# Kernel tuning notes

Hardware: AMD Instinct MI355X
Metric: run time of the kernel (lower is better)

The kernel has to match this reference:

```python
import jax, jax.numpy as jnp
import numpy as np

N = 20000      # nodes (all graphs in batch)
E = 320000     # edges (avg degree 16)
G = 16         # graphs in batch
D_IN = 32      # raw node feature dim
D_LAP = 16     # laplacian PE dim
D = 256        # d_model
H = 8          # heads
DH = D // H    # head dim
L = 2          # encoder layers
D_FF = 2 * D   # FFN hidden (FFN_layer1: d_model -> 2*d_model)
EPS = 1e-5


def _layer_norm(x, g, b):
    m = jnp.mean(x, axis=-1, keepdims=True)
    v = jnp.var(x, axis=-1, keepdims=True)
    return g * (x - m) * jax.lax.rsqrt(v + EPS) + b


def setup_inputs() -> dict:
    key = jax.random.key(0)
    ks = jax.random.split(key, 32)

    feat = jax.random.normal(ks[0], (N, D_IN), dtype=jnp.float32)
    lap_pos = jax.random.normal(ks[1], (N, D_LAP), dtype=jnp.float32)
    # random +-1 sign flip per PE dim (done with torch.rand in the original forward)
    sign_flip = jnp.where(jax.random.uniform(ks[2], (D_LAP,)) >= 0.5, 1.0, -1.0).astype(jnp.float32)

    src = jax.random.randint(ks[3], (E,), 0, N, dtype=jnp.int32)
    dst = jax.random.randint(ks[4], (E,), 0, N, dtype=jnp.int32)
    graph_ids = jnp.sort(jax.random.randint(ks[5], (N,), 0, G, dtype=jnp.int32))

    def xavier(k, shape):
        fan_in, fan_out = shape[-2], shape[-1]
        lim = np.sqrt(6.0 / (fan_in + fan_out))
        return jax.random.uniform(k, shape, minval=-lim, maxval=lim, dtype=jnp.float32)

    inp = {
        "feat": feat, "lap_pos": lap_pos, "sign_flip": sign_flip,
        "src": src, "dst": dst, "graph_ids": graph_ids,
        # input embeddings
        "Wh": xavier(ks[6], (D_IN, D)), "bh": jnp.zeros((D,), jnp.float32),
        "Wlp": xavier(ks[7], (D_LAP, D)), "blp": jnp.zeros((D,), jnp.float32),
        # per-layer params, stacked on leading layer axis
        "Wq": xavier(ks[8], (L, D, D)), "Wk": xavier(ks[9], (L, D, D)),
        "Wv": xavier(ks[10], (L, D, D)),
        "Wo": xavier(ks[11], (L, D, D)), "bo": jnp.zeros((L, D), jnp.float32),
        "g1": jnp.ones((L, D), jnp.float32), "b1": jnp.zeros((L, D), jnp.float32),
        "W1": xavier(ks[12], (L, D, D_FF)), "c1": jnp.zeros((L, D_FF), jnp.float32),
        "W2": xavier(ks[13], (L, D_FF, D)), "c2": jnp.zeros((L, D), jnp.float32),
        "g2": jnp.ones((L, D), jnp.float32), "b2": jnp.zeros((L, D), jnp.float32),
    }
    return inp


def _forward(feat, lap_pos, sign_flip, src, dst, graph_ids,
             Wh, bh, Wlp, blp, Wq, Wk, Wv, Wo, bo, g1, b1, W1, c1, W2, c2, g2, b2):
    scale = np.sqrt(DH).astype(np.float32)

    h = feat @ Wh + bh                                  # [N, D]
    h = h + (lap_pos * sign_flip[None, :]) @ Wlp + blp  # add PE embedding

    for l in range(L):
        h_in1 = h
        Q = (h @ Wq[l]).reshape(N, H, DH)
        K = (h @ Wk[l]).reshape(N, H, DH)
        V = (h @ Wv[l]).reshape(N, H, DH)

        # per-edge dot-product score, then exp(clamp(score/sqrt(dh), -5, 5))
        score = jnp.sum(K[src] * Q[dst], axis=-1)                       # [E, H]
        s = jnp.exp(jnp.clip(score / scale, -5.0, 5.0))                # [E, H]

        # segment softmax of s over incoming edges per dst node (F.softmax on mailbox)
        m = jax.ops.segment_max(s, dst, num_segments=N)                 # [N, H], -inf if no in-edges
        p = jnp.exp(s - m[dst])                                         # [E, H]
        den = jax.ops.segment_sum(p, dst, num_segments=N)               # [N, H]
        msg = jax.ops.segment_sum(p[:, :, None] * V[src], dst, num_segments=N)  # [N, H, DH]
        attn = msg / jnp.where(den > 0, den, 1.0)[:, :, None]
        attn = attn.reshape(N, D)

        h = _layer_norm(h_in1 + attn @ Wo[l] + bo[l], g1[l], b1[l])
        h_in2 = h
        ff = jax.nn.relu(h @ W1[l] + c1[l]) @ W2[l] + c2[l]
        h = _layer_norm(h_in2 + ff, g2[l], b2[l])

    # mean readout per graph
    counts = jax.ops.segment_sum(jnp.ones((N,), h.dtype), graph_ids, num_segments=G)
    sums = jax.ops.segment_sum(h, graph_ids, num_segments=G)            # [G, D]
    return sums / jnp.where(counts > 0, counts, 1.0)[:, None]


def reference(feat, lap_pos, sign_flip, src, dst, graph_ids,
              Wh, bh, Wlp, blp, Wq, Wk, Wv, Wo, bo, g1, b1, W1, c1, W2, c2, g2, b2):
    return _forward(feat, lap_pos, sign_flip, src, dst, graph_ids,
                    Wh, bh, Wlp, blp, Wq, Wk, Wv, Wo, bo, g1, b1, W1, c1, W2, c2, g2, b2)
```

## Files before the change

### kernel.cpp

```cpp
#include <hip/hip_runtime.h>
#include <hip/hip_bf16.h>

#define NN   20000
#define EE   320000
#define GG   16
#define DD   256
#define HH   8
#define DHH  32
#define LLAYERS 2
#define DFF  512
#define DIN  32
#define DLAP 16
#define RSPLITS 16

typedef __attribute__((ext_vector_type(8))) short bf16x8;
typedef __attribute__((ext_vector_type(4))) float f32x4;

__device__ __forceinline__ void gld_lds16(const void* g, void* l) {
  __builtin_amdgcn_global_load_lds((const __attribute__((address_space(1))) uint32_t*)g,
                                   (__attribute__((address_space(3))) uint32_t*)l, 16, 0, 0);
}

__device__ __forceinline__ float b2f(unsigned short s) {
  union { unsigned int i; float f; } u;
  u.i = ((unsigned int)s) << 16;
  return u.f;
}

__device__ __forceinline__ unsigned short f2bu(float f) {
  __hip_bfloat16 b = __float2bfloat16(f);
  return *(unsigned short*)&b;
}

__global__ __launch_bounds__(256) void k_embed(
    const float* __restrict__ feat, const float* __restrict__ lap,
    const float* __restrict__ sign, const float* __restrict__ Wh,
    const float* __restrict__ bh, const float* __restrict__ Wlp,
    const float* __restrict__ blp, float* __restrict__ h,
    __hip_bfloat16* __restrict__ hb) {
  int n = blockIdx.x;
  int d = threadIdx.x;
  float acc = bh[d] + blp[d];
  const float* frow = feat + (size_t)n * DIN;
  const float* lrow = lap + (size_t)n * DLAP;
#pragma unroll
  for (int k = 0; k < DIN; ++k) acc += frow[k] * Wh[k * DD + d];
#pragma unroll
  for (int k = 0; k < DLAP; ++k) acc += (lrow[k] * sign[k]) * Wlp[k * DD + d];
  h[(size_t)n * DD + d] = acc;
  hb[(size_t)n * DD + d] = __float2bfloat16(acc);
}

__global__ __launch_bounds__(256) void k_wt(
    const float* __restrict__ in, __hip_bfloat16* __restrict__ out, int K, int N) {
  __shared__ float tile[32][33];
  const float* inl = in + (size_t)blockIdx.z * K * N;
  __hip_bfloat16* outl = out + (size_t)blockIdx.z * N * K;
  int bx = blockIdx.x;
  int by = blockIdx.y;
  int tx = threadIdx.x & 31, ty = threadIdx.x >> 5;
#pragma unroll
  for (int i = 0; i < 32; i += 8)
    tile[ty + i][tx] = inl[(size_t)(by * 32 + ty + i) * N + bx * 32 + tx];
  __syncthreads();
#pragma unroll
  for (int i = 0; i < 32; i += 8)
    outl[(size_t)(bx * 32 + ty + i) * K + by * 32 + tx] = __float2bfloat16(tile[tx][ty + i]);
}

template <bool BIAS, bool RELU, bool OUTBF16>
__global__ __launch_bounds__(256) void gemm_mfma(
    const __hip_bfloat16* __restrict__ A,
    const __hip_bfloat16* __restrict__ Bt0, const __hip_bfloat16* __restrict__ Bt1,
    const __hip_bfloat16* __restrict__ Bt2,
    const float* __restrict__ bias,
    void* __restrict__ C0, void* __restrict__ C1, void* __restrict__ C2,
    int M, int Ncols, int K) {
  const __hip_bfloat16* Bt = (blockIdx.z == 0) ? Bt0 : (blockIdx.z == 1) ? Bt1 : Bt2;
  void* Cout = (blockIdx.z == 0) ? C0 : (blockIdx.z == 1) ? C1 : C2;

  __shared__ short lA[2][4][128][8];
  __shared__ short lB[2][4][128][8];

  const int t = threadIdx.x;
  const int lane = t & 63, w = t >> 6;
  const int bm = blockIdx.x * 128, bn = blockIdx.y * 128;
  const int wr = w >> 1, wc = w & 1;
  const int fr = lane & 15, fg = lane >> 4;

  f32x4 acc[4][4] = {};

  auto stage = [&](int buf, int kt) {
    const int k0 = kt * 32;
#pragma unroll
    for (int it = 0; it < 2; ++it) {
      const int cbase = it * 256 + w * 64;
      const int c = cbase + lane;
      const int g = c >> 7, r = c & 127;
      int arow = bm + r;
      if (arow >= M) arow = M - 1;
      gld_lds16(A + (size_t)arow * K + k0 + g * 8,
                (short*)lA + ((size_t)buf * 4 * 128 + cbase) * 8);
      gld_lds16(Bt + (size_t)(bn + r) * K + k0 + g * 8,
                (short*)lB + ((size_t)buf * 4 * 128 + cbase) * 8);
    }
  };

  const int nt = K >> 5;
  stage(0, 0);
  for (int kt = 0; kt < nt; ++kt) {
    const int buf = kt & 1;
    __syncthreads();
    if (kt + 1 < nt) stage(buf ^ 1, kt + 1);
    bf16x8 af[4], bfr[4];
#pragma unroll
    for (int i = 0; i < 4; ++i)
      af[i] = *(const bf16x8*)&lA[buf][fg][wr * 64 + i * 16 + fr][0];
#pragma unroll
    for (int j = 0; j < 4; ++j)
      bfr[j] = *(const bf16x8*)&lB[buf][fg][wc * 64 + j * 16 + fr][0];
#pragma unroll
    for (int i = 0; i < 4; ++i)
#pragma unroll
      for (int j = 0; j < 4; ++j)
        acc[i][j] = __builtin_amdgcn_mfma_f32_16x16x32_bf16(af[i], bfr[j], acc[i][j], 0, 0, 0);
  }

#pragma unroll
  for (int i = 0; i < 4; ++i) {
    const int row0 = bm + wr * 64 + i * 16 + fg * 4;
#pragma unroll
    for (int j = 0; j < 4; ++j) {
      const int col = bn + wc * 64 + j * 16 + fr;
      float bv = BIAS ? bias[col] : 0.f;
#pragma unroll
      for (int r = 0; r < 4; ++r) {
        const int row = row0 + r;
        if (row >= M) continue;
        float v = acc[i][j][r] + bv;
        if (RELU) v = fmaxf(v, 0.f);
        if (OUTBF16)
          ((__hip_bfloat16*)Cout)[(size_t)row * Ncols + col] = __float2bfloat16(v);
        else
          ((float*)Cout)[(size_t)row * Ncols + col] = v;
      }
    }
  }
}

__global__ void k_hist(const int* __restrict__ dst, int* __restrict__ deg, int n) {
  int i = blockIdx.x * blockDim.x + threadIdx.x;
  if (i < n) atomicAdd(&deg[dst[i]], 1);
}

__global__ __launch_bounds__(256) void k_scan_block(
    const int* __restrict__ in, int* __restrict__ ex, int* __restrict__ bsum, int n) {
  __shared__ int sm[256];
  int t = threadIdx.x;
  int i = blockIdx.x * 256 + t;
  int v = (i < n) ? in[i] : 0;
  sm[t] = v;
  __syncthreads();
  for (int o = 1; o < 256; o <<= 1) {
    int x = (t >= o) ? sm[t - o] : 0;
    __syncthreads();
    sm[t] += x;
    __syncthreads();
  }
  if (i < n) ex[i] = sm[t] - v;
  if (t == 255) bsum[blockIdx.x] = sm[255];
}

__global__ __launch_bounds__(256) void k_scan_top(
    const int* __restrict__ bsum, int* __restrict__ boff, int nb) {
  __shared__ int sm[256];
  int t = threadIdx.x;
  int v = (t < nb) ? bsum[t] : 0;
  sm[t] = v;
  __syncthreads();
  for (int o = 1; o < 256; o <<= 1) {
    int x = (t >= o) ? sm[t - o] : 0;
    __syncthreads();
    sm[t] += x;
    __syncthreads();
  }
  if (t < nb) boff[t] = sm[t] - v;
}

__global__ void k_finish_indptr(const int* __restrict__ ex, const int* __restrict__ boff,
                                int* __restrict__ indptr, int* __restrict__ cursor,
                                int n, int total) {
  int i = blockIdx.x * 256 + threadIdx.x;
  if (i < n) {
    int v = ex[i] + boff[i >> 8];
    indptr[i] = v;
    cursor[i] = v;
  }
  if (i == 0) indptr[n] = total;
}

__global__ void k_fill(const int* __restrict__ dst, const int* __restrict__ src,
                       int* __restrict__ cursor, int* __restrict__ csr_src,
                       int* __restrict__ csr_dst, int n) {
  int i = blockIdx.x * blockDim.x + threadIdx.x;
  if (i < n) {
    int d = dst[i];
    int pos = atomicAdd(&cursor[d], 1);
    csr_src[pos] = src[i];
    csr_dst[pos] = d;
  }
}

__global__ void k_bounds(const int* __restrict__ gid, int* __restrict__ gb, int n) {
  int i = blockIdx.x * blockDim.x + threadIdx.x;
  if (i >= n) return;
  int g = gid[i];
  if (i == 0) {
    for (int x = 0; x <= g; ++x) gb[x] = 0;
  } else {
    int pg = gid[i - 1];
    for (int x = pg + 1; x <= g; ++x) gb[x] = i;
  }
  if (i == n - 1) {
    for (int x = g + 1; x <= GG; ++x) gb[x] = n;
  }
}

__global__ __launch_bounds__(256) void k_edge_score(
    const __hip_bfloat16* __restrict__ Q, const __hip_bfloat16* __restrict__ Kb,
    const int* __restrict__ csr_src, const int* __restrict__ csr_dst,
    float* __restrict__ sedge, int ne) {
  int idx = blockIdx.x * blockDim.x + threadIdx.x;
  if (idx >= ne * HH) return;
  int pos = idx >> 3;
  int hh = idx & 7;
  const bf16x8* kr = (const bf16x8*)(Kb + (size_t)csr_src[pos] * DD + hh * DHH);
  const bf16x8* qr = (const bf16x8*)(Q + (size_t)csr_dst[pos] * DD + hh * DHH);
  float dot = 0.f;
#pragma unroll
  for (int c = 0; c < 4; ++c) {
    bf16x8 a = kr[c], b = qr[c];
#pragma unroll
    for (int u = 0; u < 8; ++u) dot += b2f((unsigned short)a[u]) * b2f((unsigned short)b[u]);
  }
  float x = dot * 0.17677669529663687f;
  x = fminf(fmaxf(x, -5.f), 5.f);
  sedge[idx] = expf(x);
}

__global__ __launch_bounds__(256) void k_aggregate(
    const int* __restrict__ indptr, const int* __restrict__ csr_src,
    const float* __restrict__ sedge,
    const __hip_bfloat16* __restrict__ V, __hip_bfloat16* __restrict__ attn) {
  int n = blockIdx.x * 4 + (threadIdx.x >> 6);
  if (n >= NN) return;
  int lane = threadIdx.x & 63;
  int hh = lane >> 3;
  int doff = lane * 4;
  int s0 = indptr[n], s1 = indptr[n + 1];

  float m = 0.f;
#pragma unroll 4
  for (int j = s0; j < s1; ++j) m = fmaxf(m, sedge[(size_t)j * HH + hh]);

  float den = 0.f;
  float a0 = 0.f, a1 = 0.f, a2 = 0.f, a3 = 0.f;
#pragma unroll 2
  for (int j = s0; j < s1; ++j) {
    float p = expf(sedge[(size_t)j * HH + hh] - m);
    den += p;
    int srow = csr_src[j];
    ushort4 v = *(const ushort4*)((const unsigned short*)V + (size_t)srow * DD + doff);
    a0 += p * b2f(v.x);
    a1 += p * b2f(v.y);
    a2 += p * b2f(v.z);
    a3 += p * b2f(v.w);
  }
  float inv = 1.f / (den > 0.f ? den : 1.f);
  ushort4 o;
  o.x = f2bu(a0 * inv);
  o.y = f2bu(a1 * inv);
  o.z = f2bu(a2 * inv);
  o.w = f2bu(a3 * inv);
  *(ushort4*)((unsigned short*)attn + (size_t)n * DD + doff) = o;
}

__global__ __launch_bounds__(256) void k_ln(
    float* __restrict__ h, const float* __restrict__ add,
    const float* __restrict__ g, const float* __restrict__ b,
    __hip_bfloat16* __restrict__ hb, int n) {
  int row = blockIdx.x * 4 + (threadIdx.x >> 6);
  int lane = threadIdx.x & 63;
  if (row >= n) return;
  const size_t base = (size_t)row * DD;
  float x[4];
  float s = 0.f;
#pragma unroll
  for (int j = 0; j < 4; ++j) {
    int d = lane + j * 64;
    x[j] = h[base + d] + add[base + d];
    s += x[j];
  }
#pragma unroll
  for (int o = 32; o > 0; o >>= 1) s += __shfl_xor(s, o, 64);
  float mean = s * (1.f / 256.f);
  float vs = 0.f;
#pragma unroll
  for (int j = 0; j < 4; ++j) {
    float d = x[j] - mean;
    vs += d * d;
  }
#pragma unroll
  for (int o = 32; o > 0; o >>= 1) vs += __shfl_xor(vs, o, 64);
  float rs = rsqrtf(vs * (1.f / 256.f) + 1e-5f);
#pragma unroll
  for (int j = 0; j < 4; ++j) {
    int d = lane + j * 64;
    float v = g[d] * ((x[j] - mean) * rs) + b[d];
    h[base + d] = v;
    hb[base + d] = __float2bfloat16(v);
  }
}

__global__ __launch_bounds__(256) void k_gmean(
    const float* __restrict__ h, const int* __restrict__ gb,
    float* __restrict__ gsum) {
  int g = blockIdx.x, s = blockIdx.y;
  int t = threadIdx.x;
  int r0 = gb[g], r1 = gb[g + 1];
  int len = r1 - r0;
  int per = (len + RSPLITS - 1) / RSPLITS;
  int a = r0 + s * per;
  int b = min(r1, a + per);
  if (a >= b) return;
  float acc = 0.f;
  for (int r = a; r < b; ++r) acc += h[(size_t)r * DD + t];
  atomicAdd(&gsum[g * DD + t], acc);
}

__global__ void k_final(const float* __restrict__ gsum, const int* __restrict__ gb,
                        float* __restrict__ out) {
  int g = blockIdx.x, t = threadIdx.x;
  int len = gb[g + 1] - gb[g];
  out[g * DD + t] = gsum[g * DD + t] / (len > 0 ? (float)len : 1.f);
}

extern "C" void kernel_launch(void* const* d_in, const int* in_sizes, int n_in,
                              void* d_out, int out_size, void* d_ws, size_t ws_size,
                              hipStream_t stream) {
  const float* feat = (const float*)d_in[0];
  const float* lap  = (const float*)d_in[1];
  const float* sign = (const float*)d_in[2];
  const int* srcs   = (const int*)d_in[3];
  const int* dsts   = (const int*)d_in[4];
  const int* gids   = (const int*)d_in[5];
  const float* Wh   = (const float*)d_in[6];
  const float* bh   = (const float*)d_in[7];
  const float* Wlp  = (const float*)d_in[8];
  const float* blp  = (const float*)d_in[9];
  const float* Wq   = (const float*)d_in[10];
  const float* Wk   = (const float*)d_in[11];
  const float* Wv   = (const float*)d_in[12];
  const float* Wo   = (const float*)d_in[13];
  const float* bo   = (const float*)d_in[14];
  const float* g1   = (const float*)d_in[15];
  const float* b1   = (const float*)d_in[16];
  const float* W1   = (const float*)d_in[17];
  const float* c1   = (const float*)d_in[18];
  const float* W2   = (const float*)d_in[19];
  const float* c2   = (const float*)d_in[20];
  const float* g2   = (const float*)d_in[21];
  const float* b2   = (const float*)d_in[22];

  char* base = (char*)d_ws;
  size_t off = 0;
  auto take = [&](size_t bytes) -> void* {
    void* p = base + off;
    off += (bytes + 255) & ~(size_t)255;
    return p;
  };
  float* h      = (float*)take((size_t)NN * DD * 4);
  __hip_bfloat16* hb = (__hip_bfloat16*)take((size_t)NN * DD * 2);
  __hip_bfloat16* Qb = (__hip_bfloat16*)take((size_t)NN * DD * 2);
  __hip_bfloat16* Kb = (__hip_bfloat16*)take((size_t)NN * DD * 2);
  __hip_bfloat16* Vb = (__hip_bfloat16*)take((size_t)NN * DD * 2);
  float* tmp    = (float*)take((size_t)NN * DD * 4);
  float* sedge  = (float*)take((size_t)EE * HH * 4);
  __hip_bfloat16* t1b = (__hip_bfloat16*)take((size_t)NN * DFF * 2);
  __hip_bfloat16* Wqt = (__hip_bfloat16*)take((size_t)LLAYERS * DD * DD * 2);
  __hip_bfloat16* Wkt = (__hip_bfloat16*)take((size_t)LLAYERS * DD * DD * 2);
  __hip_bfloat16* Wvt = (__hip_bfloat16*)take((size_t)LLAYERS * DD * DD * 2);
  __hip_bfloat16* Wot = (__hip_bfloat16*)take((size_t)LLAYERS * DD * DD * 2);
  __hip_bfloat16* W1t = (__hip_bfloat16*)take((size_t)LLAYERS * DD * DFF * 2);
  __hip_bfloat16* W2t = (__hip_bfloat16*)take((size_t)LLAYERS * DFF * DD * 2);
  int* deg     = (int*)take((size_t)NN * 4);
  int* ex      = (int*)take((size_t)NN * 4);
  int* bsum    = (int*)take(256 * 4);
  int* boff    = (int*)take(256 * 4);
  int* indptr  = (int*)take((size_t)(NN + 1) * 4);
  int* cursor  = (int*)take((size_t)NN * 4);
  int* csr_src = (int*)take((size_t)EE * 4);
  int* csr_dst = (int*)take((size_t)EE * 4);
  int* gb      = (int*)take((size_t)(GG + 1) * 4);
  float* gsum  = (float*)take((size_t)GG * DD * 4);
  __hip_bfloat16* attnb = Qb;

  const int NB = (NN + 255) / 256;

  k_wt<<<dim3(DD / 32, DD / 32, LLAYERS), 256, 0, stream>>>(Wq, Wqt, DD, DD);
  k_wt<<<dim3(DD / 32, DD / 32, LLAYERS), 256, 0, stream>>>(Wk, Wkt, DD, DD);
  k_wt<<<dim3(DD / 32, DD / 32, LLAYERS), 256, 0, stream>>>(Wv, Wvt, DD, DD);
  k_wt<<<dim3(DD / 32, DD / 32, LLAYERS), 256, 0, stream>>>(Wo, Wot, DD, DD);
  k_wt<<<dim3(DFF / 32, DD / 32, LLAYERS), 256, 0, stream>>>(W1, W1t, DD, DFF);
  k_wt<<<dim3(DD / 32, DFF / 32, LLAYERS), 256, 0, stream>>>(W2, W2t, DFF, DD);

  hipMemsetAsync(deg, 0, (size_t)NN * 4, stream);
  k_hist<<<(EE + 255) / 256, 256, 0, stream>>>(dsts, deg, EE);
  k_scan_block<<<NB, 256, 0, stream>>>(deg, ex, bsum, NN);
  k_scan_top<<<1, 256, 0, stream>>>(bsum, boff, NB);
  k_finish_indptr<<<NB, 256, 0, stream>>>(ex, boff, indptr, cursor, NN, EE);
  k_fill<<<(EE + 255) / 256, 256, 0, stream>>>(dsts, srcs, cursor, csr_src, csr_dst, EE);
  k_bounds<<<NB, 256, 0, stream>>>(gids, gb, NN);

  k_embed<<<NN, 256, 0, stream>>>(feat, lap, sign, Wh, bh, Wlp, blp, h, hb);

  const int MB = (NN + 127) / 128;
  dim3 gQKV(MB, DD / 128, 3);
  dim3 gD(MB, DD / 128, 1);
  dim3 gF(MB, DFF / 128, 1);

  for (int l = 0; l < LLAYERS; ++l) {
    const __hip_bfloat16* Wqt_l = Wqt + (size_t)l * DD * DD;
    const __hip_bfloat16* Wkt_l = Wkt + (size_t)l * DD * DD;
    const __hip_bfloat16* Wvt_l = Wvt + (size_t)l * DD * DD;
    const __hip_bfloat16* Wot_l = Wot + (size_t)l * DD * DD;
    const __hip_bfloat16* W1t_l = W1t + (size_t)l * DD * DFF;
    const __hip_bfloat16* W2t_l = W2t + (size_t)l * DFF * DD;
    const float* bo_l = bo + (size_t)l * DD;
    const float* g1_l = g1 + (size_t)l * DD;
    const float* b1_l = b1 + (size_t)l * DD;
    const float* c1_l = c1 + (size_t)l * DFF;
    const float* c2_l = c2 + (size_t)l * DD;
    const float* g2_l = g2 + (size_t)l * DD;
    const float* b2_l = b2 + (size_t)l * DD;

    gemm_mfma<false, false, true><<<gQKV, 256, 0, stream>>>(
        hb, Wqt_l, Wkt_l, Wvt_l, nullptr, Qb, Kb, Vb, NN, DD, DD);

    k_edge_score<<<((size_t)EE * HH + 255) / 256, 256, 0, stream>>>(
        Qb, Kb, csr_src, csr_dst, sedge, EE);
    k_aggregate<<<(NN + 3) / 4, 256, 0, stream>>>(indptr, csr_src, sedge, Vb, attnb);

    gemm_mfma<true, false, false><<<gD, 256, 0, stream>>>(
        attnb, Wot_l, Wot_l, Wot_l, bo_l, tmp, tmp, tmp, NN, DD, DD);
    k_ln<<<NN / 4, 256, 0, stream>>>(h, tmp, g1_l, b1_l, hb, NN);

    gemm_mfma<true, true, true><<<gF, 256, 0, stream>>>(
        hb, W1t_l, W1t_l, W1t_l, c1_l, t1b, t1b, t1b, NN, DFF, DD);
    gemm_mfma<true, false, false><<<gD, 256, 0, stream>>>(
        t1b, W2t_l, W2t_l, W2t_l, c2_l, tmp, tmp, tmp, NN, DD, DFF);
    k_ln<<<NN / 4, 256, 0, stream>>>(h, tmp, g2_l, b2_l, hb, NN);
  }

  hipMemsetAsync(gsum, 0, (size_t)GG * DD * 4, stream);
  k_gmean<<<dim3(GG, RSPLITS), 256, 0, stream>>>(h, gb, gsum);
  k_final<<<GG, 256, 0, stream>>>(gsum, gb, (float*)d_out);
}
```

Measured before the change: 492.6 us.

## Fuse edge scoring into online-softmax aggregation and fuse GEMM with residual LayerNorm

Edge-score and aggregation kernels are replaced by one per-node kernel that computes Q·K dot products with lane shuffles and uses an online softmax. This removes the per-edge score buffer and the csr_dst array. K and V are written interleaved into one buffer so each neighbor row is read in one place. The Wo and W2 GEMMs are fused with the residual add and LayerNorm through a 512-thread full-row tile with an LDS reduction, which drops the fp32 tmp round trip and the separate LN launches. The risk is lower occupancy in the wide GEMM and more exp calls per edge.

Result: slower. 525.4 us (+6.7%).

```diff
diff --git a/kernel.cpp b/kernel.cpp
--- a/kernel.cpp
+++ b/kernel.cpp
@@ -68,16 +68,19 @@
     outl[(size_t)(bx * 32 + ty + i) * K + by * 32 + tx] = __float2bfloat16(tile[tx][ty + i]);
 }
 
-template <bool BIAS, bool RELU, bool OUTBF16>
+template <bool BIAS, bool RELU>
 __global__ __launch_bounds__(256) void gemm_mfma(
     const __hip_bfloat16* __restrict__ A,
     const __hip_bfloat16* __restrict__ Bt0, const __hip_bfloat16* __restrict__ Bt1,
     const __hip_bfloat16* __restrict__ Bt2,
     const float* __restrict__ bias,
-    void* __restrict__ C0, void* __restrict__ C1, void* __restrict__ C2,
-    int M, int Ncols, int K) {
+    __hip_bfloat16* __restrict__ C0, __hip_bfloat16* __restrict__ C1,
+    __hip_bfloat16* __restrict__ C2,
+    int M, int K, int ldc0, int ldc12, int coff2) {
   const __hip_bfloat16* Bt = (blockIdx.z == 0) ? Bt0 : (blockIdx.z == 1) ? Bt1 : Bt2;
-  void* Cout = (blockIdx.z == 0) ? C0 : (blockIdx.z == 1) ? C1 : C2;
+  __hip_bfloat16* Cout = (blockIdx.z == 0) ? C0 : (blockIdx.z == 1) ? C1 : C2;
+  const int ldc = (blockIdx.z == 0) ? ldc0 : ldc12;
+  const int coff = (blockIdx.z == 2) ? coff2 : 0;
 
   __shared__ short lA[2][4][128][8];
   __shared__ short lB[2][4][128][8];
@@ -100,9 +103,9 @@
       int arow = bm + r;
       if (arow >= M) arow = M - 1;
       gld_lds16(A + (size_t)arow * K + k0 + g * 8,
-                (short*)lA + ((size_t)buf * 4 * 128 + cbase) * 8);
+                (short*)lA + ((size_t)buf * 512 + cbase) * 8);
       gld_lds16(Bt + (size_t)(bn + r) * K + k0 + g * 8,
-                (short*)lB + ((size_t)buf * 4 * 128 + cbase) * 8);
+                (short*)lB + ((size_t)buf * 512 + cbase) * 8);
     }
   };
 
@@ -139,10 +142,120 @@
         if (row >= M) continue;
         float v = acc[i][j][r] + bv;
         if (RELU) v = fmaxf(v, 0.f);
-        if (OUTBF16)
-          ((__hip_bfloat16*)Cout)[(size_t)row * Ncols + col] = __float2bfloat16(v);
-        else
-          ((float*)Cout)[(size_t)row * Ncols + col] = v;
+        Cout[(size_t)row * ldc + coff + col] = __float2bfloat16(v);
+      }
+    }
+  }
+}
+
+__global__ __launch_bounds__(512) void gemm_ln(
+    const __hip_bfloat16* __restrict__ A,
+    const __hip_bfloat16* __restrict__ Bt,
+    const float* __restrict__ bias,
+    float* __restrict__ h,
+    __hip_bfloat16* __restrict__ hb,
+    const float* __restrict__ g, const float* __restrict__ b,
+    int M, int K) {
+  __shared__ short lA[2][4][128][8];
+  __shared__ short lB[2][4][256][8];
+  __shared__ float redS[128];
+  __shared__ float redQ[128];
+
+  const int t = threadIdx.x;
+  const int lane = t & 63, w = t >> 6;
+  const int bm = blockIdx.x * 128;
+  const int wr = w >> 2, wc = w & 3;
+  const int fr = lane & 15, fg = lane >> 4;
+
+  if (t < 128) { redS[t] = 0.f; redQ[t] = 0.f; }
+
+  f32x4 acc[4][4] = {};
+
+  auto stage = [&](int buf, int kt) {
+    const int k0 = kt * 32;
+    {
+      const int cbase = w * 64;
+      const int c = cbase + lane;
+      const int gg = c >> 7, r = c & 127;
+      int arow = bm + r;
+      if (arow >= M) arow = M - 1;
+      gld_lds16(A + (size_t)arow * K + k0 + gg * 8,
+                (short*)lA + ((size_t)buf * 512 + cbase) * 8);
+    }
+#pragma unroll
+    for (int it = 0; it < 2; ++it) {
+      const int cbase = it * 512 + w * 64;
+      const int c = cbase + lane;
+      const int gg = c >> 8, r = c & 255;
+      gld_lds16(Bt + (size_t)r * K + k0 + gg * 8,
+                (short*)lB + ((size_t)buf * 1024 + cbase) * 8);
+    }
+  };
+
+  const int nt = K >> 5;
+  stage(0, 0);
+  for (int kt = 0; kt < nt; ++kt) {
+    const int buf = kt & 1;
+    __syncthreads();
+    if (kt + 1 < nt) stage(buf ^ 1, kt + 1);
+    bf16x8 af[4], bfr[4];
+#pragma unroll
+    for (int i = 0; i < 4; ++i)
+      af[i] = *(const bf16x8*)&lA[buf][fg][wr * 64 + i * 16 + fr][0];
+#pragma unroll
+    for (int j = 0; j < 4; ++j)
+      bfr[j] = *(const bf16x8*)&lB[buf][fg][wc * 64 + j * 16 + fr][0];
+#pragma unroll
+    for (int i = 0; i < 4; ++i)
+#pragma unroll
+      for (int j = 0; j < 4; ++j)
+        acc[i][j] = __builtin_amdgcn_mfma_f32_16x16x32_bf16(af[i], bfr[j], acc[i][j], 0, 0, 0);
+  }
+
+#pragma unroll
+  for (int i = 0; i < 4; ++i) {
+#pragma unroll
+    for (int r = 0; r < 4; ++r) {
+      const int lrow = wr * 64 + i * 16 + fg * 4 + r;
+      const int grow = bm + lrow;
+      float s = 0.f, q = 0.f;
+#pragma unroll
+      for (int j = 0; j < 4; ++j) {
+        const int col = wc * 64 + j * 16 + fr;
+        float x = acc[i][j][r] + bias[col];
+        if (grow < M) x += h[(size_t)grow * DD + col];
+        acc[i][j][r] = x;
+        s += x;
+        q += x * x;
+      }
+#pragma unroll
+      for (int o = 1; o < 16; o <<= 1) {
+        s += __shfl_xor(s, o);
+        q += __shfl_xor(q, o);
+      }
+      if (fr == 0) {
+        atomicAdd(&redS[lrow], s);
+        atomicAdd(&redQ[lrow], q);
+      }
+    }
+  }
+  __syncthreads();
+#pragma unroll
+  for (int i = 0; i < 4; ++i) {
+#pragma unroll
+    for (int r = 0; r < 4; ++r) {
+      const int lrow = wr * 64 + i * 16 + fg * 4 + r;
+      const int grow = bm + lrow;
+      if (grow >= M) continue;
+      const float mean = redS[lrow] * (1.f / 256.f);
+      const float var = redQ[lrow] * (1.f / 256.f) - mean * mean;
+      const float rs = rsqrtf(var + 1e-5f);
+#pragma unroll
+      for (int j = 0; j < 4; ++j) {
+        const int col = wc * 64 + j * 16 + fr;
+        float v = g[col] * ((acc[i][j][r] - mean) * rs) + b[col];
+        h[(size_t)grow * DD + col] = v;
+        hb[(size_t)grow * DD + col] = __float2bfloat16(v);
       }
     }
   }
@@ -200,14 +313,11 @@
 }
 
 __global__ void k_fill(const int* __restrict__ dst, const int* __restrict__ src,
-                       int* __restrict__ cursor, int* __restrict__ csr_src,
-                       int* __restrict__ csr_dst, int n) {
+                       int* __restrict__ cursor, int* __restrict__ csr_src, int n) {
   int i = blockIdx.x * blockDim.x + threadIdx.x;
   if (i < n) {
-    int d = dst[i];
-    int pos = atomicAdd(&cursor[d], 1);
+    int pos = atomicAdd(&cursor[dst[i]], 1);
     csr_src[pos] = src[i];
-    csr_dst[pos] = d;
   }
 }
 
@@ -226,55 +336,41 @@
   }
 }
 
-__global__ __launch_bounds__(256) void k_edge_score(
-    const __hip_bfloat16* __restrict__ Q, const __hip_bfloat16* __restrict__ Kb,
-    const int* __restrict__ csr_src, const int* __restrict__ csr_dst,
-    float* __restrict__ sedge, int ne) {
-  int idx = blockIdx.x * blockDim.x + threadIdx.x;
-  if (idx >= ne * HH) return;
-  int pos = idx >> 3;
-  int hh = idx & 7;
-  const bf16x8* kr = (const bf16x8*)(Kb + (size_t)csr_src[pos] * DD + hh * DHH);
-  const bf16x8* qr = (const bf16x8*)(Q + (size_t)csr_dst[pos] * DD + hh * DHH);
-  float dot = 0.f;
-#pragma unroll
-  for (int c = 0; c < 4; ++c) {
-    bf16x8 a = kr[c], b = qr[c];
-#pragma unroll
-    for (int u = 0; u < 8; ++u) dot += b2f((unsigned short)a[u]) * b2f((unsigned short)b[u]);
-  }
-  float x = dot * 0.17677669529663687f;
-  x = fminf(fmaxf(x, -5.f), 5.f);
-  sedge[idx] = expf(x);
-}
-
-__global__ __launch_bounds__(256) void k_aggregate(
+__global__ __launch_bounds__(256) void k_attn(
     const int* __restrict__ indptr, const int* __restrict__ csr_src,
-    const float* __restrict__ sedge,
-    const __hip_bfloat16* __restrict__ V, __hip_bfloat16* __restrict__ attn) {
+    const __hip_bfloat16* __restrict__ Q, const __hip_bfloat16* __restrict__ kvb,
+    __hip_bfloat16* __restrict__ attn) {
   int n = blockIdx.x * 4 + (threadIdx.x >> 6);
   if (n >= NN) return;
   int lane = threadIdx.x & 63;
-  int hh = lane >> 3;
   int doff = lane * 4;
   int s0 = indptr[n], s1 = indptr[n + 1];
 
-  float m = 0.f;
-#pragma unroll 4
-  for (int j = s0; j < s1; ++j) m = fmaxf(m, sedge[(size_t)j * HH + hh]);
-
-  float den = 0.f;
+  ushort4 qv = *(const ushort4*)((const unsigned short*)Q + (size_t)n * DD + doff);
+  float q0 = b2f(qv.x), q1 = b2f(qv.y), q2 = b2f(qv.z), q3 = b2f(qv.w);
+
+  float m = 0.f, den = 0.f;
   float a0 = 0.f, a1 = 0.f, a2 = 0.f, a3 = 0.f;
-#pragma unroll 2
   for (int j = s0; j < s1; ++j) {
-    float p = expf(sedge[(size_t)j * HH + hh] - m);
-    den += p;
     int srow = csr_src[j];
-    ushort4 v = *(const ushort4*)((const unsigned short*)V + (size_t)srow * DD + doff);
-    a0 += p * b2f(v.x);
-    a1 += p * b2f(v.y);
-    a2 += p * b2f(v.z);
-    a3 += p * b2f(v.w);
+    const unsigned short* kvrow = (const unsigned short*)kvb + (size_t)srow * (2 * DD);
+    ushort4 kv = *(const ushort4*)(kvrow + doff);
+    ushort4 vv = *(const ushort4*)(kvrow + DD + doff);
+    float dot = q0 * b2f(kv.x) + q1 * b2f(kv.y) + q2 * b2f(kv.z) + q3 * b2f(kv.w);
+    dot += __shfl_xor(dot, 1);
+    dot += __shfl_xor(dot, 2);
+    dot += __shfl_xor(dot, 4);
+    float x = fminf(fmaxf(dot * 0.17677669529663687f, -5.f), 5.f);
+    float s = expf(x);
+    float mn = fmaxf(m, s);
+    float r = expf(m - mn);
+    float p = expf(s - mn);
+    den = den * r + p;
+    a0 = a0 * r + p * b2f(vv.x);
+    a1 = a1 * r + p * b2f(vv.y);
+    a2 = a2 * r + p * b2f(vv.z);
+    a3 = a3 * r + p * b2f(vv.w);
+    m = mn;
   }
   float inv = 1.f / (den > 0.f ? den : 1.f);
   ushort4 o;
@@ -283,43 +379,6 @@
   o.z = f2bu(a2 * inv);
   o.w = f2bu(a3 * inv);
   *(ushort4*)((unsigned short*)attn + (size_t)n * DD + doff) = o;
-}
-
-__global__ __launch_bounds__(256) void k_ln(
-    float* __restrict__ h, const float* __restrict__ add,
-    const float* __restrict__ g, const float* __restrict__ b,
-    __hip_bfloat16* __restrict__ hb, int n) {
-  int row = blockIdx.x * 4 + (threadIdx.x >> 6);
-  int lane = threadIdx.x & 63;
-  if (row >= n) return;
-  const size_t base = (size_t)row * DD;
-  float x[4];
-  float s = 0.f;
-#pragma unroll
-  for (int j = 0; j < 4; ++j) {
-    int d = lane + j * 64;
-    x[j] = h[base + d] + add[base + d];
-    s += x[j];
-  }
-#pragma unroll
-  for (int o = 32; o > 0; o >>= 1) s += __shfl_xor(s, o, 64);
-  float mean = s * (1.f / 256.f);
-  float vs = 0.f;
-#pragma unroll
-  for (int j = 0; j < 4; ++j) {
-    float d = x[j] - mean;
-    vs += d * d;
-  }
-#pragma unroll
-  for (int o = 32; o > 0; o >>= 1) vs += __shfl_xor(vs, o, 64);
-  float rs = rsqrtf(vs * (1.f / 256.f) + 1e-5f);
-#pragma unroll
-  for (int j = 0; j < 4; ++j) {
-    int d = lane + j * 64;
-    float v = g[d] * ((x[j] - mean) * rs) + b[d];
-    h[base + d] = v;
-    hb[base + d] = __float2bfloat16(v);
-  }
 }
 
 __global__ __launch_bounds__(256) void k_gmean(
@@ -380,12 +439,9 @@
     return p;
   };
   float* h      = (float*)take((size_t)NN * DD * 4);
-  __hip_bfloat16* hb = (__hip_bfloat16*)take((size_t)NN * DD * 2);
-  __hip_bfloat16* Qb = (__hip_bfloat16*)take((size_t)NN * DD * 2);
-  __hip_bfloat16* Kb = (__hip_bfloat16*)take((size_t)NN * DD * 2);
-  __hip_bfloat16* Vb = (__hip_bfloat16*)take((size_t)NN * DD * 2);
-  float* tmp    = (float*)take((size_t)NN * DD * 4);
-  float* sedge  = (float*)take((size_t)EE * HH * 4);
+  __hip_bfloat16* hb  = (__hip_bfloat16*)take((size_t)NN * DD * 2);
+  __hip_bfloat16* Qb  = (__hip_bfloat16*)take((size_t)NN * DD * 2);
+  __hip_bfloat16* kvb = (__hip_bfloat16*)take((size_t)NN * 2 * DD * 2);
   __hip_bfloat16* t1b = (__hip_bfloat16*)take((size_t)NN * DFF * 2);
   __hip_bfloat16* Wqt = (__hip_bfloat16*)take((size_t)LLAYERS * DD * DD * 2);
   __hip_bfloat16* Wkt = (__hip_bfloat16*)take((size_t)LLAYERS * DD * DD * 2);
@@ -400,7 +456,6 @@
   int* indptr  = (int*)take((size_t)(NN + 1) * 4);
   int* cursor  = (int*)take((size_t)NN * 4);
   int* csr_src = (int*)take((size_t)EE * 4);
-  int* csr_dst = (int*)take((size_t)EE * 4);
   int* gb      = (int*)take((size_t)(GG + 1) * 4);
   float* gsum  = (float*)take((size_t)GG * DD * 4);
   __hip_bfloat16* attnb = Qb;
@@ -419,15 +474,15 @@
   k_scan_block<<<NB, 256, 0, stream>>>(deg, ex, bsum, NN);
   k_scan_top<<<1, 256, 0, stream>>>(bsum, boff, NB);
   k_finish_indptr<<<NB, 256, 0, stream>>>(ex, boff, indptr, cursor, NN, EE);
-  k_fill<<<(EE + 255) / 256, 256, 0, stream>>>(dsts, srcs, cursor, csr_src, csr_dst, EE);
+  k_fill<<<(EE + 255) / 256, 256, 0, stream>>>(dsts, srcs, cursor, csr_src, EE);
   k_bounds<<<NB, 256, 0, stream>>>(gids, gb, NN);
 
   k_embed<<<NN, 256, 0, stream>>>(feat, lap, sign, Wh, bh, Wlp, blp, h, hb);
 
   const int MB = (NN + 127) / 128;
   dim3 gQKV(MB, DD / 128, 3);
-  dim3 gD(MB, DD / 128, 1);
   dim3 gF(MB, DFF / 128, 1);
+  dim3 gLN(MB, 1, 1);
 
   for (int l = 0; l < LLAYERS; ++l) {
     const __hip_bfloat16* Wqt_l = Wqt + (size_t)l * DD * DD;
@@ -444,22 +499,17 @@
     const float* g2_l = g2 + (size_t)l * DD;
     const float* b2_l = b2 + (size_t)l * DD;
 
-    gemm_mfma<false, false, true><<<gQKV, 256, 0, stream>>>(
-        hb, Wqt_l, Wkt_l, Wvt_l, nullptr, Qb, Kb, Vb, NN, DD, DD);
-
-    k_edge_score<<<((size_t)EE * HH + 255) / 256, 256, 0, stream>>>(
-        Qb, Kb, csr_src, csr_dst, sedge, EE);
-    k_aggregate<<<(NN + 3) / 4, 256, 0, stream>>>(indptr, csr_src, sedge, Vb, attnb);
-
-    gemm_mfma<true, false, false><<<gD, 256, 0, stream>>>(
-        attnb, Wot_l, Wot_l, Wot_l, bo_l, tmp, tmp, tmp, NN, DD, DD);
-    k_ln<<<NN / 4, 256, 0, stream>>>(h, tmp, g1_l, b1_l, hb, NN);
-
-    gemm_mfma<true, true, true><<<gF, 256, 0, stream>>>(
-        hb, W1t_l, W1t_l, W1t_l, c1_l, t1b, t1b, t1b, NN, DFF, DD);
-    gemm_mfma<true, false, false><<<gD, 256, 0, stream>>>(
-        t1b, W2t_l, W2t_l, W2t_l, c2_l, tmp, tmp, tmp, NN, DD, DFF);
-    k_ln<<<NN / 4, 256, 0, stream>>>(h, tmp, g2_l, b2_l, hb, NN);
+    gemm_mfma<false, false><<<gQKV, 256, 0, stream>>>(
+        hb, Wqt_l, Wkt_l, Wvt_l, nullptr, Qb, kvb, kvb, NN, DD, DD, 2 * DD, DD);
+
+    k_attn<<<(NN + 3) / 4, 256, 0, stream>>>(indptr, csr_src, Qb, kvb, attnb);
+
+    gemm_ln<<<gLN, 512, 0, stream>>>(attnb, Wot_l, bo_l, h, hb, g1_l, b1_l, NN, DD);
+
+    gemm_mfma<true, true><<<gF, 256, 0, stream>>>(
+        hb, W1t_l, W1t_l, W1t_l, c1_l, t1b, t1b, t1b, NN, DD, DFF, DFF, 0);
+
+    gemm_ln<<<gLN, 512, 0, stream>>>(t1b, W2t_l, c2_l, h, hb, g2_l, b2_l, NN, DFF);
   }
 
   hipMemsetAsync(gsum, 0, (size_t)GG * DD * 4, stream);
```
